# Kernel tuning notes

Measured on AMD Instinct MI355X. Metric: run time of the kernel, lower is better.

## Reference

```python
import jax, jax.numpy as jnp
import numpy as np

N, T, C, H, W = 16, 8, 256, 14, 14
IC = 64          # inter_channels
SCALE = 32       # nearest-upsample factor (scale_s); scale_t = 1


def setup_inputs() -> dict:
    key = jax.random.key(0)
    kx, kq1, kq2, kv1, kl, ki = jax.random.split(key, 6)
    cin = C + 1
    x = jax.random.normal(kx, (N, T, C, H, W), dtype=jnp.float32)
    lam = jax.random.uniform(kl, (), dtype=jnp.float32)
    index = jax.random.randint(ki, (N,), 0, N)
    # nn.Linear default init: U(-1/sqrt(fan_in), 1/sqrt(fan_in))
    bound = 1.0 / np.sqrt(cin)
    Wq = jax.random.uniform(kq1, (IC, cin), minval=-bound, maxval=bound, dtype=jnp.float32)
    bq = jax.random.uniform(kq2, (IC,), minval=-bound, maxval=bound, dtype=jnp.float32)
    Wv = jax.random.uniform(kv1, (1, cin), minval=-bound, maxval=bound, dtype=jnp.float32)
    Wv = Wv.at[0, C].set(4.0)   # value.weight.data[0, in_channel] = 4
    bv = jnp.zeros((1,), dtype=jnp.float32)  # value.bias.data[:] = 0
    return {"x": x, "lam": lam, "index": index, "Wq": Wq, "bq": bq, "Wv": Wv, "bv": bv}


def reference(x, lam, index, Wq, bq, Wv, bv):
    n, t, c, h, w = x.shape
    ic = Wq.shape[0]
    nt, hw = n * t, h * w
    x_lam = x.reshape(nt, c, h, w)
    x_lam_ = x[index].reshape(nt, c, h, w)           # batch-shuffled partner
    lam_block = jnp.broadcast_to(lam - 0.5, (nt, 1, h, w)).astype(x.dtype)
    x_lam = jnp.concatenate([x_lam, lam_block], axis=1)     # [nt, c+1, h, w]
    x_lam_ = jnp.concatenate([x_lam_, -lam_block], axis=1)
    # linear over channel dim (equivalent to the transpose(1,3)/Linear/transpose dance)
    q = jnp.einsum('nchw,dc->ndhw', x_lam, Wq) + bq[None, :, None, None]
    k = jnp.einsum('nchw,dc->ndhw', x_lam_, Wq) + bq[None, :, None, None]
    v = jnp.einsum('nchw,dc->ndhw', x_lam_, Wv) + bv[None, :, None, None]
    q_x = q.reshape(nt, ic, hw).transpose(0, 2, 1)   # [nt, hw, ic]
    k_x = k.reshape(nt, ic, hw)                      # [nt, ic, hw]
    v_ = v.reshape(nt, 1, hw).transpose(0, 2, 1)     # [nt, hw, 1]
    scores = jnp.einsum('nqd,ndk->nqk', q_x, k_x) / jnp.sqrt(jnp.float32(ic))
    attn = jax.nn.softmax(scores, axis=-1)           # [nt, hw, hw]
    mask_lam_ = jnp.matmul(attn.astype(jnp.float32), v_.astype(jnp.float32))
    mask_lam_ = mask_lam_.reshape(nt, 1, h, w)       # scale_t == 1 so expand is a no-op
    # F.interpolate(mode='nearest', scale_factor=SCALE)
    mask_lam_ = jnp.repeat(jnp.repeat(mask_lam_, SCALE, axis=2), SCALE, axis=3)
    mask_lam_ = jax.nn.sigmoid(mask_lam_)
    mask = jnp.concatenate([1.0 - mask_lam_, mask_lam_], axis=1)  # [nt, 2, h*S, w*S]
    v_out = v_.reshape(n, t, h, w)                    # (n, t*scale_t, h, w)
    return mask, v_out
```

## Files before the change

kernel.cpp:

```cpp
#include <hip/hip_runtime.h>
#include <hip/hip_bf16.h>
#include <stdint.h>

#define HWsz 196
#define MASK_ELEMS 51380224
#define VOUT_OFF   MASK_ELEMS

#define EQ_OFF_F 3221504
#define EK_OFF_F 4024704
#define V_OFF    4827904

typedef __attribute__((ext_vector_type(8))) short short8;
typedef __attribute__((ext_vector_type(4))) short short4v;
typedef __attribute__((ext_vector_type(4))) float f32x4;

__device__ __forceinline__ bool is_bf16_mode(const void* wv) {
  return ((const uint16_t*)wv)[256] == (uint16_t)0x4080;
}

__device__ __forceinline__ float ldf(const void* p, int i, bool bf) {
  if (bf) {
    uint32_t u = (uint32_t)((const uint16_t*)p)[i] << 16;
    return __builtin_bit_cast(float, u);
  }
  return ((const float*)p)[i];
}

__device__ __forceinline__ uint16_t f2bf(float f) {
  __hip_bfloat16 h = __float2bfloat16(f);
  return __builtin_bit_cast(uint16_t, h);
}

__device__ __forceinline__ float bf2f(uint16_t u) {
  uint32_t v = (uint32_t)u << 16;
  return __builtin_bit_cast(float, v);
}

template<int NMT, int NCOLS, int J0>
__device__ __forceinline__ void k1_body(uint16_t* Abuf,
    const void* xraw, const int* index, const void* Wqraw, const void* bqraw,
    const void* Wvraw, const void* bvraw, const void* lamraw,
    float* ws, void* dout, int b) {
  int s = b & 127, isK = (b >> 7) & 1;
  int src = isK ? index[s >> 3] * 8 + (s & 7) : s;
  bool bf = is_bf16_mode(Wvraw);
  int tid = threadIdx.x;
  int lane = tid & 63, w = tid >> 6;
  int ln = lane & 15, quad = lane >> 4;
  int d = w * 16 + ln;
  size_t xbase = (size_t)src * 256 * 196;

  f32x4 acc[NMT];
#pragma unroll
  for (int mt = 0; mt < NMT; mt++) acc[mt] = (f32x4){0.f, 0.f, 0.f, 0.f};
  int cS1 = tid >> 2, jjS1 = tid & 3;
  uint32_t abase = (uint32_t)(uintptr_t)Abuf + (uint32_t)(quad * 128);

#pragma unroll 1
  for (int chunk = 0; chunk < 4; chunk++) {
    short8 bw0, bw1;
    {
      int cb = d * 257 + chunk * 64 + quad * 8;
#pragma unroll
      for (int e = 0; e < 8; e++) {
        bw0[e] = (short)f2bf(ldf(Wqraw, cb + e, bf));
        bw1[e] = (short)f2bf(ldf(Wqraw, cb + 32 + e, bf));
      }
    }
    __syncthreads();
    if (bf) {
      const uint16_t* xp = (const uint16_t*)xraw + xbase +
                           (size_t)(chunk * 64 + cS1) * 196 + J0;
      for (int jj = jjS1; jj * 4 < NCOLS; jj += 4)
        *(uint2*)(Abuf + (jj >> 2) * 1024 + cS1 * 16 + (jj & 3) * 4) =
            *(const uint2*)(xp + jj * 4);
    } else {
      const float* xp = (const float*)xraw + xbase +
                        (size_t)(chunk * 64 + cS1) * 196 + J0;
      for (int jj = jjS1; jj * 4 < NCOLS; jj += 4) {
        float4 v4 = *(const float4*)(xp + jj * 4);
        uint2 pk;
        pk.x = (uint32_t)f2bf(v4.x) | ((uint32_t)f2bf(v4.y) << 16);
        pk.y = (uint32_t)f2bf(v4.z) | ((uint32_t)f2bf(v4.w) << 16);
        *(uint2*)(Abuf + (jj >> 2) * 1024 + cS1 * 16 + (jj & 3) * 4) = pk;
      }
    }
    __syncthreads();
#pragma unroll
    for (int kc2 = 0; kc2 < 2; kc2++) {
      short4v lo[NMT], hi[NMT];
#pragma unroll
      for (int mt = 0; mt < NMT; mt++) {
        asm volatile("ds_read_b64_tr_b16 %0, %2 offset:%3\n\t"
                     "ds_read_b64_tr_b16 %1, %2 offset:%4"
                     : "=v"(lo[mt]), "=v"(hi[mt])
                     : "v"(abase), "i"(mt * 2048 + kc2 * 1024),
                       "i"(mt * 2048 + kc2 * 1024 + 128));
      }
      asm volatile("s_waitcnt lgkmcnt(0)" ::: "memory");
      __builtin_amdgcn_sched_barrier(0);
#pragma unroll
      for (int mt = 0; mt < NMT; mt++) {
        short8 af = __builtin_shufflevector(lo[mt], hi[mt], 0, 1, 2, 3, 4, 5, 6, 7);
        acc[mt] = __builtin_amdgcn_mfma_f32_16x16x32_bf16(af, kc2 ? bw1 : bw0,
                                                          acc[mt], 0, 0, 0);
      }
    }
  }

  float lamv = ldf(lamraw, 0, bf) - 0.5f;
  float lamch = isK ? -lamv : lamv;
  float addend = ldf(Wqraw, d * 257 + 256, bf) * lamch + ldf(bqraw, d, bf);
  uint16_t* E = (uint16_t*)(ws + (isK ? EK_OFF_F : EQ_OFF_F));
#pragma unroll
  for (int mt = 0; mt < NMT; mt++) {
#pragma unroll
    for (int r = 0; r < 4; r++) {
      int j = J0 + mt * 16 + quad * 4 + r;
      if (j < HWsz) E[((size_t)s * HWsz + j) * 64 + d] = f2bf(acc[mt][r] + addend);
    }
  }

  if (isK && tid < NCOLS) {
    int j = J0 + tid;
    float vp0 = 0.f, vp1 = 0.f, vp2 = 0.f, vp3 = 0.f;
    if (bf) {
      const uint16_t* xp = (const uint16_t*)xraw + xbase + j;
#pragma unroll 4
      for (int c = 0; c < 256; c += 4) {
        vp0 = fmaf(bf2f(xp[(size_t)(c + 0) * 196]), ldf(Wvraw, c + 0, bf), vp0);
        vp1 = fmaf(bf2f(xp[(size_t)(c + 1) * 196]), ldf(Wvraw, c + 1, bf), vp1);
        vp2 = fmaf(bf2f(xp[(size_t)(c + 2) * 196]), ldf(Wvraw, c + 2, bf), vp2);
        vp3 = fmaf(bf2f(xp[(size_t)(c + 3) * 196]), ldf(Wvraw, c + 3, bf), vp3);
      }
    } else {
      const float* xp = (const float*)xraw + xbase + j;
#pragma unroll 4
      for (int c = 0; c < 256; c += 4) {
        vp0 = fmaf(xp[(size_t)(c + 0) * 196], ldf(Wvraw, c + 0, bf), vp0);
        vp1 = fmaf(xp[(size_t)(c + 1) * 196], ldf(Wvraw, c + 1, bf), vp1);
        vp2 = fmaf(xp[(size_t)(c + 2) * 196], ldf(Wvraw, c + 2, bf), vp2);
        vp3 = fmaf(xp[(size_t)(c + 3) * 196], ldf(Wvraw, c + 3, bf), vp3);
      }
    }
    float vvv = (vp0 + vp1) + (vp2 + vp3) + ldf(Wvraw, 256, bf) * lamch + ldf(bvraw, 0, bf);
    ws[V_OFF + s * HWsz + j] = vvv;
    if (bf) ((uint16_t*)dout)[VOUT_OFF + s * HWsz + j] = f2bf(vvv);
    else    ((float*)dout)[VOUT_OFF + s * HWsz + j] = vvv;
  }
}

__global__ __launch_bounds__(256) void k1_qk(const void* xraw, const int* index,
    const void* Wqraw, const void* bqraw, const void* Wvraw, const void* bvraw,
    const void* lamraw, float* ws, void* dout) {
  __shared__ __align__(16) uint16_t Abuf[7 * 1024];
  int b = blockIdx.x;
  if (b < 256)
    k1_body<7, 112, 0>(Abuf, xraw, index, Wqraw, bqraw, Wvraw, bvraw, lamraw, ws, dout, b);
  else
    k1_body<6, 84, 112>(Abuf, xraw, index, Wqraw, bqraw, Wvraw, bvraw, lamraw, ws, dout, b & 255);
}

__global__ __launch_bounds__(256) void k2_attn_mask(float* ws, void* dout, const void* Wvraw) {
  __shared__ float sig[64];
  bool bf = is_bf16_mode(Wvraw);
  int s = blockIdx.x >> 2, blk = blockIdx.x & 3;
  int tid = threadIdx.x;
  int lane = tid & 63, w = tid >> 6;
  int mt = blk * 4 + w;
  int ln = lane & 15, quad = lane >> 4;

  if (mt < 13) {
    const uint16_t* Eq = (const uint16_t*)(ws + EQ_OFF_F);
    const uint16_t* Ek = (const uint16_t*)(ws + EK_OFF_F);
    const uint16_t* qrow = Eq + ((size_t)s * 196 + mt * 16 + ln) * 64 + quad * 8;
    short8 aq0 = *(const short8*)(qrow);
    short8 aq1 = *(const short8*)(qrow + 32);

    float vcol[13];
    f32x4 acc[13];
#pragma unroll
    for (int nt = 0; nt < 13; nt++) {
      int col = nt * 16 + ln;
      vcol[nt] = (col < 196) ? ws[V_OFF + s * 196 + col] : 0.f;
      const uint16_t* krow = Ek + ((size_t)s * 196 + col) * 64 + quad * 8;
      short8 b0 = *(const short8*)(krow);
      short8 b1 = *(const short8*)(krow + 32);
      f32x4 a = (f32x4){0.f, 0.f, 0.f, 0.f};
      a = __builtin_amdgcn_mfma_f32_16x16x32_bf16(aq0, b0, a, 0, 0, 0);
      a = __builtin_amdgcn_mfma_f32_16x16x32_bf16(aq1, b1, a, 0, 0, 0);
      acc[nt] = a;
    }

    float mx[4] = {-1e30f, -1e30f, -1e30f, -1e30f};
#pragma unroll
    for (int nt = 0; nt < 13; nt++) {
      bool valid = (nt * 16 + ln) < 196;
#pragma unroll
      for (int r = 0; r < 4; r++) {
        float sv = valid ? acc[nt][r] * 0.125f : -1e30f;
        acc[nt][r] = sv;
        mx[r] = fmaxf(mx[r], sv);
      }
    }
#pragma unroll
    for (int m = 1; m < 16; m <<= 1)
#pragma unroll
      for (int r = 0; r < 4; r++) mx[r] = fmaxf(mx[r], __shfl_xor(mx[r], m));

    float l[4] = {0.f, 0.f, 0.f, 0.f}, av[4] = {0.f, 0.f, 0.f, 0.f};
#pragma unroll
    for (int nt = 0; nt < 13; nt++)
#pragma unroll
      for (int r = 0; r < 4; r++) {
        float p = __expf(acc[nt][r] - mx[r]);
        l[r] += p;
        av[r] += p * vcol[nt];
      }
#pragma unroll
    for (int m = 1; m < 16; m <<= 1)
#pragma unroll
      for (int r = 0; r < 4; r++) {
        l[r] += __shfl_xor(l[r], m);
        av[r] += __shfl_xor(av[r], m);
      }

    if (ln == 0) {
#pragma unroll
      for (int r = 0; r < 4; r++) {
        int j = mt * 16 + quad * 4 + r;
        if (j < 196) {
          float mval = av[r] / l[r];
          sig[j & 63] = 1.f / (1.f + __expf(-mval));
        }
      }
    }
  }
  __syncthreads();

  int j0 = blk * 64;
  int nrows = (blk == 3) ? 4 : 64;
  int base2 = s * 2;
  if (!bf) {
    float4* o4 = (float4*)dout;
    int total = nrows << 8;
    for (int i = tid; i < total; i += 256) {
      int x2 = i & 3, dy = (i >> 2) & 31, ch = (i >> 7) & 1, jl = i >> 8;
      int j = j0 + jl;
      int yhw = j / 14, xhw = j - yhw * 14;
      float v = sig[jl];
      if (!ch) v = 1.f - v;
      size_t off4 = (size_t)(base2 + ch) * 50176 +
                    (size_t)(yhw * 32 + dy) * 112 + (xhw << 3) + (x2 << 1);
      float4 f = make_float4(v, v, v, v);
      o4[off4] = f;
      o4[off4 + 1] = f;
    }
  } else {
    uint4* o = (uint4*)dout;
    int total = nrows << 7;
    for (int i = tid; i < total; i += 256) {
      int x2 = i & 1, dy = (i >> 1) & 31, ch = (i >> 6) & 1, jl = i >> 7;
      int j = j0 + jl;
      int yhw = j / 14, xhw = j - yhw * 14;
      float v = sig[jl];
      if (!ch) v = 1.f - v;
      uint32_t ub = (uint32_t)f2bf(v), pk = ub | (ub << 16);
      uint4 qv; qv.x = pk; qv.y = pk; qv.z = pk; qv.w = pk;
      size_t off = (size_t)(base2 + ch) * 25088 +
                   (size_t)(yhw * 32 + dy) * 56 + (xhw << 2) + (x2 << 1);
      o[off] = qv;
      o[off + 1] = qv;
    }
  }
}

extern "C" void kernel_launch(void* const* d_in, const int* in_sizes, int n_in,
                              void* d_out, int out_size, void* d_ws, size_t ws_size,
                              hipStream_t stream) {
  const void* x   = d_in[0];
  const void* lam = d_in[1];
  const int* idx  = (const int*)d_in[2];
  const void* Wq  = d_in[3];
  const void* bq  = d_in[4];
  const void* Wv  = d_in[5];
  const void* bv  = d_in[6];
  float* ws = (float*)d_ws;

  k1_qk<<<512, 256, 0, stream>>>(x, idx, Wq, bq, Wv, bv, lam, ws, d_out);
  k2_attn_mask<<<512, 256, 0, stream>>>(ws, d_out, Wv);
}
```

Measured before the change: 265.7 us.

## Prefetch x chunks into registers, fuse V projection, stage E stores, nontemporal mask writes

k1 now prefetches the next 64-channel chunk of x into registers while the MFMAs run on the current chunk. It also computes the value projection from the bf16 tile already in LDS, where before it re-read x from global memory with strided loads. The Q/K output is staged through LDS so the global stores are coalesced 16-byte writes, and the bf16/fp32 mode becomes a template parameter. k2 writes the large upsampled mask with nontemporal stores to keep it out of the cache. The costs are more registers for the prefetch buffers, extra barriers, and the value projection now using bf16-rounded x in fp32 mode, which may change accuracy slightly.

```diff
diff --git a/kernel.cpp b/kernel.cpp
--- a/kernel.cpp
+++ b/kernel.cpp
@@ -13,6 +13,7 @@
 typedef __attribute__((ext_vector_type(8))) short short8;
 typedef __attribute__((ext_vector_type(4))) short short4v;
 typedef __attribute__((ext_vector_type(4))) float f32x4;
+typedef __attribute__((ext_vector_type(4))) uint32_t u32x4;
 
 __device__ __forceinline__ bool is_bf16_mode(const void* wv) {
   return ((const uint16_t*)wv)[256] == (uint16_t)0x4080;
@@ -36,14 +37,13 @@
   return __builtin_bit_cast(float, v);
 }
 
-template<int NMT, int NCOLS, int J0>
+template<int NMT, int NCOLS, int J0, bool BF>
 __device__ __forceinline__ void k1_body(uint16_t* Abuf,
     const void* xraw, const int* index, const void* Wqraw, const void* bqraw,
     const void* Wvraw, const void* bvraw, const void* lamraw,
     float* ws, void* dout, int b) {
   int s = b & 127, isK = (b >> 7) & 1;
   int src = isK ? index[s >> 3] * 8 + (s & 7) : s;
-  bool bf = is_bf16_mode(Wvraw);
   int tid = threadIdx.x;
   int lane = tid & 63, w = tid >> 6;
   int ln = lane & 15, quad = lane >> 4;
@@ -53,8 +53,31 @@
   f32x4 acc[NMT];
 #pragma unroll
   for (int mt = 0; mt < NMT; mt++) acc[mt] = (f32x4){0.f, 0.f, 0.f, 0.f};
+  float vacc = 0.f;
   int cS1 = tid >> 2, jjS1 = tid & 3;
+  int vdB = (tid >> 4) * 1024 + (tid & 15);
   uint32_t abase = (uint32_t)(uintptr_t)Abuf + (uint32_t)(quad * 128);
+
+  float4 r32[7];
+  uint2  r16[7];
+
+  {
+    if constexpr (BF) {
+      const uint16_t* xp = (const uint16_t*)xraw + xbase + (size_t)cS1 * 196 + J0;
+#pragma unroll
+      for (int u = 0; u < 7; u++) {
+        int jj = jjS1 + u * 4;
+        if (jj * 4 < NCOLS) r16[u] = *(const uint2*)(xp + jj * 4);
+      }
+    } else {
+      const float* xp = (const float*)xraw + xbase + (size_t)cS1 * 196 + J0;
+#pragma unroll
+      for (int u = 0; u < 7; u++) {
+        int jj = jjS1 + u * 4;
+        if (jj * 4 < NCOLS) r32[u] = *(const float4*)(xp + jj * 4);
+      }
+    }
+  }
 
 #pragma unroll 1
   for (int chunk = 0; chunk < 4; chunk++) {
@@ -63,29 +86,45 @@
       int cb = d * 257 + chunk * 64 + quad * 8;
 #pragma unroll
       for (int e = 0; e < 8; e++) {
-        bw0[e] = (short)f2bf(ldf(Wqraw, cb + e, bf));
-        bw1[e] = (short)f2bf(ldf(Wqraw, cb + 32 + e, bf));
+        bw0[e] = (short)f2bf(ldf(Wqraw, cb + e, BF));
+        bw1[e] = (short)f2bf(ldf(Wqraw, cb + 32 + e, BF));
+      }
+    }
+    if (chunk) __syncthreads();
+#pragma unroll
+    for (int u = 0; u < 7; u++) {
+      int jj = jjS1 + u * 4;
+      if (jj * 4 < NCOLS) {
+        uint2 pk;
+        if constexpr (BF) pk = r16[u];
+        else {
+          float4 v4 = r32[u];
+          pk.x = (uint32_t)f2bf(v4.x) | ((uint32_t)f2bf(v4.y) << 16);
+          pk.y = (uint32_t)f2bf(v4.z) | ((uint32_t)f2bf(v4.w) << 16);
+        }
+        *(uint2*)(Abuf + (jj >> 2) * 1024 + cS1 * 16 + (jj & 3) * 4) = pk;
       }
     }
     __syncthreads();
-    if (bf) {
-      const uint16_t* xp = (const uint16_t*)xraw + xbase +
-                           (size_t)(chunk * 64 + cS1) * 196 + J0;
-      for (int jj = jjS1; jj * 4 < NCOLS; jj += 4)
-        *(uint2*)(Abuf + (jj >> 2) * 1024 + cS1 * 16 + (jj & 3) * 4) =
-            *(const uint2*)(xp + jj * 4);
-    } else {
-      const float* xp = (const float*)xraw + xbase +
-                        (size_t)(chunk * 64 + cS1) * 196 + J0;
-      for (int jj = jjS1; jj * 4 < NCOLS; jj += 4) {
-        float4 v4 = *(const float4*)(xp + jj * 4);
-        uint2 pk;
-        pk.x = (uint32_t)f2bf(v4.x) | ((uint32_t)f2bf(v4.y) << 16);
-        pk.y = (uint32_t)f2bf(v4.z) | ((uint32_t)f2bf(v4.w) << 16);
-        *(uint2*)(Abuf + (jj >> 2) * 1024 + cS1 * 16 + (jj & 3) * 4) = pk;
-      }
-    }
-    __syncthreads();
+    if (chunk < 3) {
+      if constexpr (BF) {
+        const uint16_t* xp = (const uint16_t*)xraw + xbase +
+                             (size_t)((chunk + 1) * 64 + cS1) * 196 + J0;
+#pragma unroll
+        for (int u = 0; u < 7; u++) {
+          int jj = jjS1 + u * 4;
+          if (jj * 4 < NCOLS) r16[u] = *(const uint2*)(xp + jj * 4);
+        }
+      } else {
+        const float* xp = (const float*)xraw + xbase +
+                          (size_t)((chunk + 1) * 64 + cS1) * 196 + J0;
+#pragma unroll
+        for (int u = 0; u < 7; u++) {
+          int jj = jjS1 + u * 4;
+          if (jj * 4 < NCOLS) r32[u] = *(const float4*)(xp + jj * 4);
+        }
+      }
+    }
 #pragma unroll
     for (int kc2 = 0; kc2 < 2; kc2++) {
       short4v lo[NMT], hi[NMT];
@@ -106,46 +145,38 @@
                                                           acc[mt], 0, 0, 0);
       }
     }
-  }
-
-  float lamv = ldf(lamraw, 0, bf) - 0.5f;
+    if (isK && tid < NCOLS) {
+#pragma unroll 8
+      for (int c = 0; c < 64; c++)
+        vacc = fmaf(bf2f(Abuf[vdB + c * 16]), ldf(Wvraw, chunk * 64 + c, BF), vacc);
+    }
+  }
+
+  float lamv = ldf(lamraw, 0, BF) - 0.5f;
   float lamch = isK ? -lamv : lamv;
-  float addend = ldf(Wqraw, d * 257 + 256, bf) * lamch + ldf(bqraw, d, bf);
-  uint16_t* E = (uint16_t*)(ws + (isK ? EK_OFF_F : EQ_OFF_F));
+  float addend = ldf(Wqraw, d * 257 + 256, BF) * lamch + ldf(bqraw, d, BF);
+  __syncthreads();
 #pragma unroll
   for (int mt = 0; mt < NMT; mt++) {
 #pragma unroll
     for (int r = 0; r < 4; r++) {
-      int j = J0 + mt * 16 + quad * 4 + r;
-      if (j < HWsz) E[((size_t)s * HWsz + j) * 64 + d] = f2bf(acc[mt][r] + addend);
-    }
+      int jl = mt * 16 + quad * 4 + r;
+      if (jl < NCOLS) Abuf[jl * 64 + d] = f2bf(acc[mt][r] + addend);
+    }
+  }
+  __syncthreads();
+  {
+    uint16_t* E = (uint16_t*)(ws + (isK ? EK_OFF_F : EQ_OFF_F));
+    const u32x4* As4 = (const u32x4*)Abuf;
+    u32x4* Eg4 = (u32x4*)(E + (size_t)(s * HWsz + J0) * 64);
+    for (int i = tid; i < NCOLS * 8; i += 256) Eg4[i] = As4[i];
   }
 
   if (isK && tid < NCOLS) {
     int j = J0 + tid;
-    float vp0 = 0.f, vp1 = 0.f, vp2 = 0.f, vp3 = 0.f;
-    if (bf) {
-      const uint16_t* xp = (const uint16_t*)xraw + xbase + j;
-#pragma unroll 4
-      for (int c = 0; c < 256; c += 4) {
-        vp0 = fmaf(bf2f(xp[(size_t)(c + 0) * 196]), ldf(Wvraw, c + 0, bf), vp0);
-        vp1 = fmaf(bf2f(xp[(size_t)(c + 1) * 196]), ldf(Wvraw, c + 1, bf), vp1);
-        vp2 = fmaf(bf2f(xp[(size_t)(c + 2) * 196]), ldf(Wvraw, c + 2, bf), vp2);
-        vp3 = fmaf(bf2f(xp[(size_t)(c + 3) * 196]), ldf(Wvraw, c + 3, bf), vp3);
-      }
-    } else {
-      const float* xp = (const float*)xraw + xbase + j;
-#pragma unroll 4
-      for (int c = 0; c < 256; c += 4) {
-        vp0 = fmaf(xp[(size_t)(c + 0) * 196], ldf(Wvraw, c + 0, bf), vp0);
-        vp1 = fmaf(xp[(size_t)(c + 1) * 196], ldf(Wvraw, c + 1, bf), vp1);
-        vp2 = fmaf(xp[(size_t)(c + 2) * 196], ldf(Wvraw, c + 2, bf), vp2);
-        vp3 = fmaf(xp[(size_t)(c + 3) * 196], ldf(Wvraw, c + 3, bf), vp3);
-      }
-    }
-    float vvv = (vp0 + vp1) + (vp2 + vp3) + ldf(Wvraw, 256, bf) * lamch + ldf(bvraw, 0, bf);
+    float vvv = vacc + ldf(Wvraw, 256, BF) * lamch + ldf(bvraw, 0, BF);
     ws[V_OFF + s * HWsz + j] = vvv;
-    if (bf) ((uint16_t*)dout)[VOUT_OFF + s * HWsz + j] = f2bf(vvv);
+    if (BF) ((uint16_t*)dout)[VOUT_OFF + s * HWsz + j] = f2bf(vvv);
     else    ((float*)dout)[VOUT_OFF + s * HWsz + j] = vvv;
   }
 }
@@ -155,10 +186,14 @@
     const void* lamraw, float* ws, void* dout) {
   __shared__ __align__(16) uint16_t Abuf[7 * 1024];
   int b = blockIdx.x;
-  if (b < 256)
-    k1_body<7, 112, 0>(Abuf, xraw, index, Wqraw, bqraw, Wvraw, bvraw, lamraw, ws, dout, b);
-  else
-    k1_body<6, 84, 112>(Abuf, xraw, index, Wqraw, bqraw, Wvraw, bvraw, lamraw, ws, dout, b & 255);
+  bool bf = is_bf16_mode(Wvraw);
+  if (b < 256) {
+    if (bf) k1_body<7, 112, 0, true >(Abuf, xraw, index, Wqraw, bqraw, Wvraw, bvraw, lamraw, ws, dout, b);
+    else    k1_body<7, 112, 0, false>(Abuf, xraw, index, Wqraw, bqraw, Wvraw, bvraw, lamraw, ws, dout, b);
+  } else {
+    if (bf) k1_body<6, 84, 112, true >(Abuf, xraw, index, Wqraw, bqraw, Wvraw, bvraw, lamraw, ws, dout, b & 255);
+    else    k1_body<6, 84, 112, false>(Abuf, xraw, index, Wqraw, bqraw, Wvraw, bvraw, lamraw, ws, dout, b & 255);
+  }
 }
 
 __global__ __launch_bounds__(256) void k2_attn_mask(float* ws, void* dout, const void* Wvraw) {
@@ -242,7 +277,7 @@
   int nrows = (blk == 3) ? 4 : 64;
   int base2 = s * 2;
   if (!bf) {
-    float4* o4 = (float4*)dout;
+    f32x4* o4 = (f32x4*)dout;
     int total = nrows << 8;
     for (int i = tid; i < total; i += 256) {
       int x2 = i & 3, dy = (i >> 2) & 31, ch = (i >> 7) & 1, jl = i >> 8;
@@ -252,12 +287,12 @@
       if (!ch) v = 1.f - v;
       size_t off4 = (size_t)(base2 + ch) * 50176 +
                     (size_t)(yhw * 32 + dy) * 112 + (xhw << 3) + (x2 << 1);
-      float4 f = make_float4(v, v, v, v);
-      o4[off4] = f;
-      o4[off4 + 1] = f;
+      f32x4 f = (f32x4){v, v, v, v};
+      __builtin_nontemporal_store(f, &o4[off4]);
+      __builtin_nontemporal_store(f, &o4[off4 + 1]);
     }
   } else {
-    uint4* o = (uint4*)dout;
+    u32x4* o = (u32x4*)dout;
     int total = nrows << 7;
     for (int i = tid; i < total; i += 256) {
       int x2 = i & 1, dy = (i >> 1) & 31, ch = (i >> 6) & 1, jl = i >> 7;
@@ -266,11 +301,11 @@
       float v = sig[jl];
       if (!ch) v = 1.f - v;
       uint32_t ub = (uint32_t)f2bf(v), pk = ub | (ub << 16);
-      uint4 qv; qv.x = pk; qv.y = pk; qv.z = pk; qv.w = pk;
+      u32x4 qv = (u32x4){pk, pk, pk, pk};
       size_t off = (size_t)(base2 + ch) * 25088 +
                    (size_t)(yhw * 32 + dy) * 56 + (xhw << 2) + (x2 << 1);
-      o[off] = qv;
-      o[off + 1] = qv;
+      __builtin_nontemporal_store(qv, &o[off]);
+      __builtin_nontemporal_store(qv, &o[off + 1]);
     }
   }
 }
```

Result: slower. 297.4 us (+11.9%).
